# Optimization experiments

Hardware: AMD Instinct MI355X
Metric: run time of the kernel (lower is better)

## Reference

```python
import jax, jax.numpy as jnp
import numpy as np

N_HEADS = 16

def setup_inputs() -> dict:
    key = jax.random.key(0)
    ks = jax.random.split(key, 5)
    B, T, D, L = 2, 2048, 1024, 128
    x = jax.random.normal(ks[0], (B, T, D), dtype=jnp.float32)
    w_q = jax.random.normal(ks[1], (D, D), dtype=jnp.float32) / np.sqrt(D)
    w_d = jax.random.normal(ks[2], (D, L), dtype=jnp.float32) / np.sqrt(D)
    w_k = jax.random.normal(ks[3], (L, D), dtype=jnp.float32) / np.sqrt(L)
    w_v = jax.random.normal(ks[4], (L, D), dtype=jnp.float32) / np.sqrt(L)
    mask = jnp.ones((B, T), dtype=jnp.int32)
    return {"x": x, "mask": mask, "w_q": w_q, "w_d": w_d, "w_k": w_k, "w_v": w_v}


def reference(x, mask, w_q, w_d, w_k, w_v):
    B, T, D = x.shape
    H = N_HEADS
    dh = D // H
    q = x @ w_q                      # [B,T,D]
    latent = x @ w_d                 # [B,T,L]
    k = latent @ w_k                 # [B,T,D]
    v = latent @ w_v                 # [B,T,D]

    def split(t):
        return t.reshape(B, T, H, dh).transpose(0, 2, 1, 3)  # [B,H,T,dh]

    q, k, v = split(q), split(k), split(v)
    scores = jnp.einsum('bhqd,bhkd->bhqk', q, k) / jnp.sqrt(jnp.float32(dh))
    causal = jnp.tril(jnp.ones((T, T), dtype=bool))          # [T,T]
    keep = causal[None, None, :, :] & (mask[:, None, None, :] != 0)
    scores = jnp.where(keep, scores, jnp.float32(-jnp.inf))
    probs = jax.nn.softmax(scores, axis=-1)
    out = jnp.einsum('bhqk,bhkd->bhqd', probs, v)            # [B,H,T,dh]
    return out.transpose(0, 2, 1, 3).reshape(B, T, D)
```

## Files before the change

### kernel.cpp

```cpp
#include <hip/hip_runtime.h>

typedef __attribute__((ext_vector_type(8))) short bf16x8;
typedef __attribute__((ext_vector_type(4))) float f32x4;
typedef __attribute__((ext_vector_type(4))) unsigned u32x4;

__device__ inline unsigned short f2bf(float f) {
  unsigned u = __builtin_bit_cast(unsigned, f);
  unsigned r = u + 0x7FFFu + ((u >> 16) & 1u);
  return (unsigned short)(r >> 16);
}
__device__ inline float bf2f(unsigned short s) {
  unsigned u = ((unsigned)s) << 16;
  return __builtin_bit_cast(float, u);
}
__device__ inline float fexp2(float x) { return __builtin_amdgcn_exp2f(x); }

__device__ inline void gload_lds16(const unsigned short* g, unsigned short* l) {
  __builtin_amdgcn_global_load_lds(
      (const __attribute__((address_space(1))) unsigned int*)g,
      (__attribute__((address_space(3))) unsigned int*)l, 16, 0, 0);
}

__device__ __host__ inline int pv_perm(int k) {
  return ((k >> 5) & 1) * 32 + ((k >> 2) & 3) * 8 + ((k >> 4) & 1) * 4 + (k & 3);
}

__global__ __launch_bounds__(256) void prep_kernel(
    const float* __restrict__ x, const int* __restrict__ mask,
    const float* __restrict__ w_q, const float* __restrict__ w_d,
    const float* __restrict__ w_k, const float* __restrict__ w_v,
    unsigned short* __restrict__ x_bf, unsigned short* __restrict__ wqdt,
    unsigned short* __restrict__ wkvt, float* __restrict__ bias,
    int* __restrict__ tileok) {
  int bid = blockIdx.x;
  if (bid < 1024) {
    int base = bid * 4096 + threadIdx.x * 4;
#pragma unroll
    for (int it = 0; it < 4; ++it) {
      int idx = base + it * 1024;
      float4 v = *(const float4*)&x[idx];
      ushort4 o;
      o.x = f2bf(v.x); o.y = f2bf(v.y); o.z = f2bf(v.z); o.w = f2bf(v.w);
      *(ushort4*)&x_bf[idx] = o;
    }
    return;
  }
  int tb = bid - 1024;
  if (tb >= 1408) {
    int i = (tb - 1408) * 256 + threadIdx.x;
    int mv = mask[i];
    bias[i] = mv ? 0.0f : -1e30f;
    int ok = __all(mv != 0);
    if ((threadIdx.x & 63) == 0) tileok[i >> 6] = ok;
    return;
  }
  const float* in; unsigned short* out; int R, C, tr, tc;
  if (tb < 1024)      { in = w_q; out = wqdt;               R = 1024; C = 1024; tr = tb >> 5; tc = tb & 31; }
  else if (tb < 1152) { int t2 = tb - 1024; in = w_d; out = wqdt + 1024 * 1024; R = 1024; C = 128; tr = t2 >> 2; tc = t2 & 3; }
  else if (tb < 1280) { int t2 = tb - 1152; in = w_k; out = wkvt;               R = 128; C = 1024; tr = t2 >> 5; tc = t2 & 31; }
  else                { int t2 = tb - 1280; in = w_v; out = wkvt + 1024 * 128;  R = 128; C = 1024; tr = t2 >> 5; tc = t2 & 31; }
  __shared__ float t[32][33];
  int r0 = tr * 32, c0 = tc * 32;
  int tx = threadIdx.x & 31, ty = threadIdx.x >> 5;
  for (int r = ty; r < 32; r += 8)
    t[r][tx] = in[(size_t)(r0 + r) * C + c0 + tx];
  __syncthreads();
  for (int cc = ty; cc < 32; cc += 8)
    out[(size_t)(c0 + cc) * R + r0 + tx] = f2bf(t[tx][cc]);
}

template <int BN>
__global__ __launch_bounds__(256) void gemm_bt(const unsigned short* __restrict__ A, int lda,
                                               const unsigned short* __restrict__ Bt, int ldb,
                                               unsigned short* __restrict__ C, int ldc,
                                               int K) {
  constexpr int WM = (BN == 128) ? 2 : 4;
  constexpr int WN = 4 / WM;
  constexpr int MR = 128 / WM / 16;
  constexpr int NR = BN / WN / 16;
  constexpr int RPW = 128 / WM;
  constexpr int CPW = BN / WN;
  __shared__ unsigned short As[128 * 32];
  __shared__ unsigned short Bs[BN * 32];
  int m0 = blockIdx.x * 128, n0 = blockIdx.y * BN;
  int tid = threadIdx.x, w = tid >> 6, l = tid & 63;
  int lr = l & 15, lg = l >> 4;
  int wr = w / WN, wc = w % WN;
  f32x4 acc[MR][NR] = {};

  for (int k0 = 0; k0 < K; k0 += 32) {
    __syncthreads();
#pragma unroll
    for (int it = 0; it < 2; ++it) {
      int c = w * 2 + it;
      int row = c * 16 + (l >> 2);
      int col = (l & 3) * 8;
      gload_lds16(&A[(size_t)(m0 + row) * lda + k0 + col], &As[c * 512 + l * 8]);
    }
    if constexpr (BN == 128) {
#pragma unroll
      for (int it = 0; it < 2; ++it) {
        int c = w * 2 + it;
        int row = c * 16 + (l >> 2);
        int col = (l & 3) * 8;
        gload_lds16(&Bt[(size_t)(n0 + row) * ldb + k0 + col], &Bs[c * 512 + l * 8]);
      }
    } else {
      int row = w * 16 + (l >> 2);
      int col = (l & 3) * 8;
      gload_lds16(&Bt[(size_t)(n0 + row) * ldb + k0 + col], &Bs[w * 512 + l * 8]);
    }
    __syncthreads();
    bf16x8 af[MR], bfr[NR];
#pragma unroll
    for (int m = 0; m < MR; ++m)
      af[m] = *(const bf16x8*)&As[(wr * RPW + m * 16 + lr) * 32 + lg * 8];
#pragma unroll
    for (int n = 0; n < NR; ++n)
      bfr[n] = *(const bf16x8*)&Bs[(wc * CPW + n * 16 + lr) * 32 + lg * 8];
    __builtin_amdgcn_s_setprio(1);
#pragma unroll
    for (int m = 0; m < MR; ++m)
#pragma unroll
      for (int n = 0; n < NR; ++n)
        acc[m][n] = __builtin_amdgcn_mfma_f32_16x16x32_bf16(af[m], bfr[n], acc[m][n], 0, 0, 0);
    __builtin_amdgcn_s_setprio(0);
  }

#pragma unroll
  for (int m = 0; m < MR; ++m)
#pragma unroll
    for (int n = 0; n < NR; ++n)
#pragma unroll
      for (int i = 0; i < 4; ++i)
        C[(size_t)(m0 + wr * RPW + m * 16 + lg * 4 + i) * ldc + n0 + wc * CPW + n * 16 + lr] =
            f2bf(acc[m][n][i]);
}

__global__ __launch_bounds__(256) void gemm_kv(const unsigned short* __restrict__ A,
                                               const unsigned short* __restrict__ Bt,
                                               unsigned short* __restrict__ kvK,
                                               unsigned short* __restrict__ vt) {
  __shared__ unsigned short As[128 * 32];
  __shared__ unsigned short Bs[128 * 32];
  int m0 = blockIdx.x * 128, n0 = blockIdx.y * 128;
  int tid = threadIdx.x, w = tid >> 6, l = tid & 63;
  int lr = l & 15, lg = l >> 4;
  int wr = w >> 1, wc = w & 1;
  f32x4 acc[4][4] = {};

  for (int k0 = 0; k0 < 128; k0 += 32) {
    __syncthreads();
#pragma unroll
    for (int it = 0; it < 2; ++it) {
      int c = w * 2 + it;
      int row = c * 16 + (l >> 2);
      int col = (l & 3) * 8;
      gload_lds16(&A[(size_t)(m0 + row) * 1152 + k0 + col], &As[c * 512 + l * 8]);
      gload_lds16(&Bt[(size_t)(n0 + row) * 128 + k0 + col], &Bs[c * 512 + l * 8]);
    }
    __syncthreads();
    bf16x8 af[4], bfr[4];
#pragma unroll
    for (int m = 0; m < 4; ++m)
      af[m] = *(const bf16x8*)&As[(wr * 64 + m * 16 + lr) * 32 + lg * 8];
#pragma unroll
    for (int n = 0; n < 4; ++n)
      bfr[n] = *(const bf16x8*)&Bs[(wc * 64 + n * 16 + lr) * 32 + lg * 8];
    __builtin_amdgcn_s_setprio(1);
#pragma unroll
    for (int m = 0; m < 4; ++m)
#pragma unroll
      for (int n = 0; n < 4; ++n)
        acc[m][n] = __builtin_amdgcn_mfma_f32_16x16x32_bf16(af[m], bfr[n], acc[m][n], 0, 0, 0);
    __builtin_amdgcn_s_setprio(0);
  }

  if (blockIdx.y < 8) {
#pragma unroll
    for (int m = 0; m < 4; ++m)
#pragma unroll
      for (int n = 0; n < 4; ++n)
#pragma unroll
        for (int i = 0; i < 4; ++i)
          kvK[(size_t)(m0 + wr * 64 + m * 16 + lg * 4 + i) * 2048 + n0 + wc * 64 + n * 16 + lr] =
              f2bf(acc[m][n][i]);
  } else {
#pragma unroll
    for (int m = 0; m < 4; ++m)
#pragma unroll
      for (int n = 0; n < 4; ++n) {
        int vc = n0 - 1024 + wc * 64 + n * 16 + lr;
        int hh = vc >> 6, dd = vc & 63;
        int row0 = m0 + wr * 64 + m * 16 + lg * 4;
        int bb = row0 >> 11, t0 = row0 & 2047;
        size_t vrow = (size_t)((bb * 16 + hh) * 64 + dd);
        int slot = (t0 >> 6) * 64 + pv_perm(t0 & 63);
        ushort4 o;
        o.x = f2bf(acc[m][n][0]); o.y = f2bf(acc[m][n][1]);
        o.z = f2bf(acc[m][n][2]); o.w = f2bf(acc[m][n][3]);
        *(ushort4*)&vt[vrow * 2048 + slot] = o;
      }
  }
}

__global__ __launch_bounds__(512, 2) void attn_kernel(const unsigned short* __restrict__ qg,
                                                      const unsigned short* __restrict__ kvg,
                                                      const unsigned short* __restrict__ vtg,
                                                      const float* __restrict__ biasg,
                                                      const int* __restrict__ tileokg,
                                                      float* __restrict__ outg) {
  const int bh = blockIdx.x, qh = blockIdx.y;
  const int b = bh >> 4, h = bh & 15;
  const int tid = threadIdx.x, w = tid >> 6, l = tid & 63;
  const int lr = l & 15, lg = l >> 4;
  const int srow = tid >> 3, sc8 = (tid & 7) * 8;

  __shared__ unsigned short Ks[2][64 * 72];
  __shared__ unsigned short Vs[2][64 * 72];

  const float QSCALE = 0.125f * 1.44269504089f;

  for (int bi = 0; bi < 2; ++bi) {
    const int band = bi ? (15 - qh) : qh;
    const int NT = 2 * band + 2;
    const int qrow0 = band * 128 + w * 16;

    bf16x8 qf[2];
#pragma unroll
    for (int ks = 0; ks < 2; ++ks) {
      bf16x8 raw = *(const bf16x8*)&qg[(size_t)(b * 2048 + qrow0 + lr) * 1152 + h * 64 + ks * 32 + lg * 8];
#pragma unroll
      for (int j = 0; j < 8; ++j)
        raw[j] = (short)f2bf(bf2f((unsigned short)raw[j]) * QSCALE);
      qf[ks] = raw;
    }

    f32x4 acc[4] = {};
    float m_i = -1e30f, l_part = 0.f;

    bf16x8 kreg = *(const bf16x8*)&kvg[(size_t)(b * 2048 + srow) * 2048 + h * 64 + sc8];
    bf16x8 vreg = *(const bf16x8*)&vtg[((size_t)(bh * 64 + srow)) * 2048 + sc8];
    __syncthreads();
    *(bf16x8*)&Ks[0][srow * 72 + sc8] = kreg;
    *(bf16x8*)&Vs[0][srow * 72 + sc8] = vreg;
    __syncthreads();
    int cur = 0;

    for (int kt = 0; kt < NT; ++kt) {
      if (kt + 1 < NT) {
        kreg = *(const bf16x8*)&kvg[(size_t)(b * 2048 + (kt + 1) * 64 + srow) * 2048 + h * 64 + sc8];
        vreg = *(const bf16x8*)&vtg[((size_t)(bh * 64 + srow)) * 2048 + (kt + 1) * 64 + sc8];
      }

      const int d = kt - 2 * band;
      const bool skip = (d == 1) && (w < 4);
      if (!skip) {
        const bool isdiag = (d == 0 && w < 4) || (d == 1 && w >= 4);
        const int dlim = (w & 3) * 16 + lr;

        f32x4 s[4];
        __builtin_amdgcn_s_setprio(1);
#pragma unroll
        for (int n = 0; n < 4; ++n) {
          bf16x8 kf0 = *(const bf16x8*)&Ks[cur][(n * 16 + lr) * 72 + lg * 8];
          bf16x8 kf1 = *(const bf16x8*)&Ks[cur][(n * 16 + lr) * 72 + 32 + lg * 8];
          f32x4 z = {};
          z = __builtin_amdgcn_mfma_f32_16x16x32_bf16(kf0, qf[0], z, 0, 0, 0);
          z = __builtin_amdgcn_mfma_f32_16x16x32_bf16(kf1, qf[1], z, 0, 0, 0);
          s[n] = z;
        }
        __builtin_amdgcn_s_setprio(0);

        const int tok = tileokg[b * 32 + kt];
        float mx = -1e30f;
        if (tok) {
          if (isdiag) {
#pragma unroll
            for (int n = 0; n < 4; ++n)
#pragma unroll
              for (int i = 0; i < 4; ++i) {
                float v = (n * 16 + lg * 4 + i <= dlim) ? s[n][i] : -1e30f;
                s[n][i] = v;
                mx = fmaxf(mx, v);
              }
          } else {
#pragma unroll
            for (int n = 0; n < 4; ++n)
#pragma unroll
              for (int i = 0; i < 4; ++i)
                mx = fmaxf(mx, s[n][i]);
          }
        } else {
#pragma unroll
          for (int n = 0; n < 4; ++n)
#pragma unroll
            for (int i = 0; i < 4; ++i) {
              int keyl = n * 16 + lg * 4 + i;
              float v = s[n][i] + biasg[b * 2048 + kt * 64 + keyl];
              if (isdiag) v = (keyl <= dlim) ? v : -1e30f;
              s[n][i] = v;
              mx = fmaxf(mx, v);
            }
        }
        mx = fmaxf(mx, __shfl_xor(mx, 16, 64));
        mx = fmaxf(mx, __shfl_xor(mx, 32, 64));

        if (__any(mx - m_i > 8.0f)) {
          float mn = fmaxf(m_i, mx);
          float sc = fexp2(m_i - mn);
          m_i = mn;
          l_part *= sc;
          float scb[4];
#pragma unroll
          for (int i = 0; i < 4; ++i) scb[i] = __shfl(sc, lg * 4 + i, 64);
#pragma unroll
          for (int dt = 0; dt < 4; ++dt)
#pragma unroll
            for (int i = 0; i < 4; ++i) acc[dt][i] *= scb[i];
        }

        float rs = 0.f;
#pragma unroll
        for (int n = 0; n < 4; ++n)
#pragma unroll
          for (int i = 0; i < 4; ++i) {
            float e = fexp2(s[n][i] - m_i);
            s[n][i] = e;
            rs += e;
          }
        l_part += rs;

        unsigned pk[4][2];
#pragma unroll
        for (int n = 0; n < 4; ++n) {
          asm("v_cvt_pk_bf16_f32 %0, %1, %2" : "=v"(pk[n][0]) : "v"(s[n][0]), "v"(s[n][1]));
          asm("v_cvt_pk_bf16_f32 %0, %1, %2" : "=v"(pk[n][1]) : "v"(s[n][2]), "v"(s[n][3]));
        }
        bf16x8 paf[2];
#pragma unroll
        for (int ks = 0; ks < 2; ++ks) {
          u32x4 uv;
          uv[0] = pk[2 * ks][0];
          uv[1] = pk[2 * ks][1];
          uv[2] = pk[2 * ks + 1][0];
          uv[3] = pk[2 * ks + 1][1];
          paf[ks] = __builtin_bit_cast(bf16x8, uv);
        }

        __builtin_amdgcn_s_setprio(1);
#pragma unroll
        for (int ks = 0; ks < 2; ++ks)
#pragma unroll
          for (int dt = 0; dt < 4; ++dt) {
            bf16x8 vf = *(const bf16x8*)&Vs[cur][(dt * 16 + lr) * 72 + ks * 32 + lg * 8];
            acc[dt] = __builtin_amdgcn_mfma_f32_16x16x32_bf16(paf[ks], vf, acc[dt], 0, 0, 0);
          }
        __builtin_amdgcn_s_setprio(0);
      }

      if (kt + 1 < NT) {
        *(bf16x8*)&Ks[cur ^ 1][srow * 72 + sc8] = kreg;
        *(bf16x8*)&Vs[cur ^ 1][srow * 72 + sc8] = vreg;
        __syncthreads();
        cur ^= 1;
      }
    }

    float lt = l_part;
    lt += __shfl_xor(lt, 16, 64);
    lt += __shfl_xor(lt, 32, 64);
    float inv = 1.f / lt;
    float invb[4];
#pragma unroll
    for (int i = 0; i < 4; ++i) invb[i] = __shfl(inv, lg * 4 + i, 64);
#pragma unroll
    for (int dt = 0; dt < 4; ++dt)
#pragma unroll
      for (int i = 0; i < 4; ++i)
        outg[(size_t)(b * 2048 + qrow0 + lg * 4 + i) * 1024 + h * 64 + dt * 16 + lr] =
            acc[dt][i] * invb[i];
  }
}

extern "C" void kernel_launch(void* const* d_in, const int* in_sizes, int n_in,
                              void* d_out, int out_size, void* d_ws, size_t ws_size,
                              hipStream_t stream) {
  const float* x    = (const float*)d_in[0];
  const int*   mask = (const int*)d_in[1];
  const float* w_q  = (const float*)d_in[2];
  const float* w_d  = (const float*)d_in[3];
  const float* w_k  = (const float*)d_in[4];
  const float* w_v  = (const float*)d_in[5];
  float* out = (float*)d_out;

  char* ws = (char*)d_ws;
  size_t off = 0;
  auto alloc = [&](size_t elems) {
    unsigned short* p = (unsigned short*)(ws + off);
    off += ((elems * 2 + 255) & ~(size_t)255);
    return p;
  };
  unsigned short* x_bf = alloc(4194304);
  unsigned short* wqdt = alloc(1152 * 1024);
  unsigned short* wkvt = alloc(2048 * 128);
  unsigned short* qlat = alloc(4096 * 1152);
  unsigned short* kv   = alloc(4096 * 2048);
  unsigned short* vt   = alloc(4194304);
  float* bias = (float*)alloc(8192);
  int* tileok = (int*)alloc(128);

  prep_kernel<<<2448, 256, 0, stream>>>(x, mask, w_q, w_d, w_k, w_v, x_bf, wqdt, wkvt, bias, tileok);

  gemm_bt<64><<<dim3(32, 18), 256, 0, stream>>>(x_bf, 1024, wqdt, 1024, qlat, 1152, 1024);
  gemm_kv<<<dim3(32, 16), 256, 0, stream>>>(qlat + 1024, wkvt, kv, vt);

  attn_kernel<<<dim3(32, 8), 512, 0, stream>>>(qlat, kv, vt, bias, tileok, out);
}
```

Measured before the change: 84.23 us.

## Shrink attention blocks to 64-row bands and deepen Q-GEMM K-step

The attention kernel now uses 256-thread blocks, each handling two paired 64-row query bands instead of two 128-row bands, on a grid twice as large. This removes the wasted half-diagonal tile and the per-wave skip logic, and it balances causal work in finer pieces. Each thread now stages two K/V chunks per tile. The Q-projection GEMM is specialised into gemm_q, which loads a 64-wide K slab per sync (two 32-wide LDS panels) to halve the number of barriers. The cost is extra LDS use and more register pressure.

```diff
diff --git a/kernel.cpp b/kernel.cpp
--- a/kernel.cpp
+++ b/kernel.cpp
@@ -69,71 +69,59 @@
     out[(size_t)(c0 + cc) * R + r0 + tx] = f2bf(t[tx][cc]);
 }
 
-template <int BN>
-__global__ __launch_bounds__(256) void gemm_bt(const unsigned short* __restrict__ A, int lda,
-                                               const unsigned short* __restrict__ Bt, int ldb,
-                                               unsigned short* __restrict__ C, int ldc,
-                                               int K) {
-  constexpr int WM = (BN == 128) ? 2 : 4;
-  constexpr int WN = 4 / WM;
-  constexpr int MR = 128 / WM / 16;
-  constexpr int NR = BN / WN / 16;
-  constexpr int RPW = 128 / WM;
-  constexpr int CPW = BN / WN;
-  __shared__ unsigned short As[128 * 32];
-  __shared__ unsigned short Bs[BN * 32];
-  int m0 = blockIdx.x * 128, n0 = blockIdx.y * BN;
+__global__ __launch_bounds__(256) void gemm_q(const unsigned short* __restrict__ A,
+                                              const unsigned short* __restrict__ Bt,
+                                              unsigned short* __restrict__ C) {
+  __shared__ unsigned short As[2][128 * 32];
+  __shared__ unsigned short Bs[2][64 * 32];
+  int m0 = blockIdx.x * 128, n0 = blockIdx.y * 64;
   int tid = threadIdx.x, w = tid >> 6, l = tid & 63;
   int lr = l & 15, lg = l >> 4;
-  int wr = w / WN, wc = w % WN;
-  f32x4 acc[MR][NR] = {};
-
-  for (int k0 = 0; k0 < K; k0 += 32) {
-    __syncthreads();
+  f32x4 acc[2][4] = {};
+
+  for (int k0 = 0; k0 < 1024; k0 += 64) {
+    __syncthreads();
+#pragma unroll
+    for (int it = 0; it < 4; ++it) {
+      int s = w * 4 + it;
+      int p = s >> 3, c = s & 7;
+      int row = c * 16 + (l >> 2), col = (l & 3) * 8;
+      gload_lds16(&A[(size_t)(m0 + row) * 1024 + k0 + p * 32 + col], &As[p][c * 512 + l * 8]);
+    }
 #pragma unroll
     for (int it = 0; it < 2; ++it) {
-      int c = w * 2 + it;
-      int row = c * 16 + (l >> 2);
-      int col = (l & 3) * 8;
-      gload_lds16(&A[(size_t)(m0 + row) * lda + k0 + col], &As[c * 512 + l * 8]);
-    }
-    if constexpr (BN == 128) {
-#pragma unroll
-      for (int it = 0; it < 2; ++it) {
-        int c = w * 2 + it;
-        int row = c * 16 + (l >> 2);
-        int col = (l & 3) * 8;
-        gload_lds16(&Bt[(size_t)(n0 + row) * ldb + k0 + col], &Bs[c * 512 + l * 8]);
-      }
-    } else {
-      int row = w * 16 + (l >> 2);
-      int col = (l & 3) * 8;
-      gload_lds16(&Bt[(size_t)(n0 + row) * ldb + k0 + col], &Bs[w * 512 + l * 8]);
-    }
-    __syncthreads();
-    bf16x8 af[MR], bfr[NR];
-#pragma unroll
-    for (int m = 0; m < MR; ++m)
-      af[m] = *(const bf16x8*)&As[(wr * RPW + m * 16 + lr) * 32 + lg * 8];
-#pragma unroll
-    for (int n = 0; n < NR; ++n)
-      bfr[n] = *(const bf16x8*)&Bs[(wc * CPW + n * 16 + lr) * 32 + lg * 8];
-    __builtin_amdgcn_s_setprio(1);
-#pragma unroll
-    for (int m = 0; m < MR; ++m)
-#pragma unroll
-      for (int n = 0; n < NR; ++n)
-        acc[m][n] = __builtin_amdgcn_mfma_f32_16x16x32_bf16(af[m], bfr[n], acc[m][n], 0, 0, 0);
-    __builtin_amdgcn_s_setprio(0);
-  }
-
-#pragma unroll
-  for (int m = 0; m < MR; ++m)
-#pragma unroll
-    for (int n = 0; n < NR; ++n)
+      int s = w * 2 + it;
+      int p = s >> 2, c = s & 3;
+      int row = c * 16 + (l >> 2), col = (l & 3) * 8;
+      gload_lds16(&Bt[(size_t)(n0 + row) * 1024 + k0 + p * 32 + col], &Bs[p][c * 512 + l * 8]);
+    }
+    __syncthreads();
+#pragma unroll
+    for (int p = 0; p < 2; ++p) {
+      bf16x8 af[2], bfr[4];
+#pragma unroll
+      for (int m = 0; m < 2; ++m)
+        af[m] = *(const bf16x8*)&As[p][(w * 32 + m * 16 + lr) * 32 + lg * 8];
+#pragma unroll
+      for (int n = 0; n < 4; ++n)
+        bfr[n] = *(const bf16x8*)&Bs[p][(n * 16 + lr) * 32 + lg * 8];
+      __builtin_amdgcn_s_setprio(1);
+#pragma unroll
+      for (int m = 0; m < 2; ++m)
+#pragma unroll
+        for (int n = 0; n < 4; ++n)
+          acc[m][n] = __builtin_amdgcn_mfma_f32_16x16x32_bf16(af[m], bfr[n], acc[m][n], 0, 0, 0);
+      __builtin_amdgcn_s_setprio(0);
+    }
+  }
+
+#pragma unroll
+  for (int m = 0; m < 2; ++m)
+#pragma unroll
+    for (int n = 0; n < 4; ++n)
 #pragma unroll
       for (int i = 0; i < 4; ++i)
-        C[(size_t)(m0 + wr * RPW + m * 16 + lg * 4 + i) * ldc + n0 + wc * CPW + n * 16 + lr] =
+        C[(size_t)(m0 + w * 32 + m * 16 + lg * 4 + i) * 1152 + n0 + n * 16 + lr] =
             f2bf(acc[m][n][i]);
 }
 
@@ -204,17 +192,16 @@
   }
 }
 
-__global__ __launch_bounds__(512, 2) void attn_kernel(const unsigned short* __restrict__ qg,
+__global__ __launch_bounds__(256, 2) void attn_kernel(const unsigned short* __restrict__ qg,
                                                       const unsigned short* __restrict__ kvg,
                                                       const unsigned short* __restrict__ vtg,
                                                       const float* __restrict__ biasg,
                                                       const int* __restrict__ tileokg,
                                                       float* __restrict__ outg) {
-  const int bh = blockIdx.x, qh = blockIdx.y;
+  const int bh = blockIdx.x, pr = blockIdx.y;
   const int b = bh >> 4, h = bh & 15;
   const int tid = threadIdx.x, w = tid >> 6, l = tid & 63;
   const int lr = l & 15, lg = l >> 4;
-  const int srow = tid >> 3, sc8 = (tid & 7) * 8;
 
   __shared__ unsigned short Ks[2][64 * 72];
   __shared__ unsigned short Vs[2][64 * 72];
@@ -222,9 +209,9 @@
   const float QSCALE = 0.125f * 1.44269504089f;
 
   for (int bi = 0; bi < 2; ++bi) {
-    const int band = bi ? (15 - qh) : qh;
-    const int NT = 2 * band + 2;
-    const int qrow0 = band * 128 + w * 16;
+    const int band = bi ? (31 - pr) : pr;
+    const int NT = band + 1;
+    const int qrow0 = band * 64 + w * 16;
 
     bf16x8 qf[2];
 #pragma unroll
@@ -239,129 +226,142 @@
     f32x4 acc[4] = {};
     float m_i = -1e30f, l_part = 0.f;
 
-    bf16x8 kreg = *(const bf16x8*)&kvg[(size_t)(b * 2048 + srow) * 2048 + h * 64 + sc8];
-    bf16x8 vreg = *(const bf16x8*)&vtg[((size_t)(bh * 64 + srow)) * 2048 + sc8];
-    __syncthreads();
-    *(bf16x8*)&Ks[0][srow * 72 + sc8] = kreg;
-    *(bf16x8*)&Vs[0][srow * 72 + sc8] = vreg;
+    bf16x8 kreg[2], vreg[2];
+#pragma unroll
+    for (int it = 0; it < 2; ++it) {
+      int slot = it * 256 + tid, row = slot >> 3, c8 = (slot & 7) * 8;
+      kreg[it] = *(const bf16x8*)&kvg[(size_t)(b * 2048 + row) * 2048 + h * 64 + c8];
+      vreg[it] = *(const bf16x8*)&vtg[((size_t)(bh * 64 + row)) * 2048 + c8];
+    }
+    __syncthreads();
+#pragma unroll
+    for (int it = 0; it < 2; ++it) {
+      int slot = it * 256 + tid, row = slot >> 3, c8 = (slot & 7) * 8;
+      *(bf16x8*)&Ks[0][row * 72 + c8] = kreg[it];
+      *(bf16x8*)&Vs[0][row * 72 + c8] = vreg[it];
+    }
     __syncthreads();
     int cur = 0;
 
     for (int kt = 0; kt < NT; ++kt) {
       if (kt + 1 < NT) {
-        kreg = *(const bf16x8*)&kvg[(size_t)(b * 2048 + (kt + 1) * 64 + srow) * 2048 + h * 64 + sc8];
-        vreg = *(const bf16x8*)&vtg[((size_t)(bh * 64 + srow)) * 2048 + (kt + 1) * 64 + sc8];
-      }
-
-      const int d = kt - 2 * band;
-      const bool skip = (d == 1) && (w < 4);
-      if (!skip) {
-        const bool isdiag = (d == 0 && w < 4) || (d == 1 && w >= 4);
-        const int dlim = (w & 3) * 16 + lr;
-
-        f32x4 s[4];
-        __builtin_amdgcn_s_setprio(1);
-#pragma unroll
-        for (int n = 0; n < 4; ++n) {
-          bf16x8 kf0 = *(const bf16x8*)&Ks[cur][(n * 16 + lr) * 72 + lg * 8];
-          bf16x8 kf1 = *(const bf16x8*)&Ks[cur][(n * 16 + lr) * 72 + 32 + lg * 8];
-          f32x4 z = {};
-          z = __builtin_amdgcn_mfma_f32_16x16x32_bf16(kf0, qf[0], z, 0, 0, 0);
-          z = __builtin_amdgcn_mfma_f32_16x16x32_bf16(kf1, qf[1], z, 0, 0, 0);
-          s[n] = z;
+#pragma unroll
+        for (int it = 0; it < 2; ++it) {
+          int slot = it * 256 + tid, row = slot >> 3, c8 = (slot & 7) * 8;
+          kreg[it] = *(const bf16x8*)&kvg[(size_t)(b * 2048 + (kt + 1) * 64 + row) * 2048 + h * 64 + c8];
+          vreg[it] = *(const bf16x8*)&vtg[((size_t)(bh * 64 + row)) * 2048 + (kt + 1) * 64 + c8];
         }
-        __builtin_amdgcn_s_setprio(0);
-
-        const int tok = tileokg[b * 32 + kt];
-        float mx = -1e30f;
-        if (tok) {
-          if (isdiag) {
-#pragma unroll
-            for (int n = 0; n < 4; ++n)
-#pragma unroll
-              for (int i = 0; i < 4; ++i) {
-                float v = (n * 16 + lg * 4 + i <= dlim) ? s[n][i] : -1e30f;
-                s[n][i] = v;
-                mx = fmaxf(mx, v);
-              }
-          } else {
-#pragma unroll
-            for (int n = 0; n < 4; ++n)
-#pragma unroll
-              for (int i = 0; i < 4; ++i)
-                mx = fmaxf(mx, s[n][i]);
-          }
-        } else {
+      }
+
+      const bool diag = (kt == NT - 1);
+      const int dlim = w * 16 + lr;
+
+      f32x4 s[4];
+      __builtin_amdgcn_s_setprio(1);
+#pragma unroll
+      for (int n = 0; n < 4; ++n) {
+        bf16x8 kf0 = *(const bf16x8*)&Ks[cur][(n * 16 + lr) * 72 + lg * 8];
+        bf16x8 kf1 = *(const bf16x8*)&Ks[cur][(n * 16 + lr) * 72 + 32 + lg * 8];
+        f32x4 z = {};
+        z = __builtin_amdgcn_mfma_f32_16x16x32_bf16(kf0, qf[0], z, 0, 0, 0);
+        z = __builtin_amdgcn_mfma_f32_16x16x32_bf16(kf1, qf[1], z, 0, 0, 0);
+        s[n] = z;
+      }
+      __builtin_amdgcn_s_setprio(0);
+
+      const int tok = tileokg[b * 32 + kt];
+      float mx = -1e30f;
+      if (tok) {
+        if (diag) {
 #pragma unroll
           for (int n = 0; n < 4; ++n)
 #pragma unroll
             for (int i = 0; i < 4; ++i) {
-              int keyl = n * 16 + lg * 4 + i;
-              float v = s[n][i] + biasg[b * 2048 + kt * 64 + keyl];
-              if (isdiag) v = (keyl <= dlim) ? v : -1e30f;
+              float v = (n * 16 + lg * 4 + i <= dlim) ? s[n][i] : -1e30f;
               s[n][i] = v;
               mx = fmaxf(mx, v);
             }
+        } else {
+#pragma unroll
+          for (int n = 0; n < 4; ++n)
+#pragma unroll
+            for (int i = 0; i < 4; ++i)
+              mx = fmaxf(mx, s[n][i]);
         }
-        mx = fmaxf(mx, __shfl_xor(mx, 16, 64));
-        mx = fmaxf(mx, __shfl_xor(mx, 32, 64));
-
-        if (__any(mx - m_i > 8.0f)) {
-          float mn = fmaxf(m_i, mx);
-          float sc = fexp2(m_i - mn);
-          m_i = mn;
-          l_part *= sc;
-          float scb[4];
-#pragma unroll
-          for (int i = 0; i < 4; ++i) scb[i] = __shfl(sc, lg * 4 + i, 64);
-#pragma unroll
-          for (int dt = 0; dt < 4; ++dt)
-#pragma unroll
-            for (int i = 0; i < 4; ++i) acc[dt][i] *= scb[i];
+      } else {
+#pragma unroll
+        for (int n = 0; n < 4; ++n)
+#pragma unroll
+          for (int i = 0; i < 4; ++i) {
+            int keyl = n * 16 + lg * 4 + i;
+            float v = s[n][i] + biasg[b * 2048 + kt * 64 + keyl];
+            if (diag) v = (keyl <= dlim) ? v : -1e30f;
+            s[n][i] = v;
+            mx = fmaxf(mx, v);
+          }
+      }
+      mx = fmaxf(mx, __shfl_xor(mx, 16, 64));
+      mx = fmaxf(mx, __shfl_xor(mx, 32, 64));
+
+      if (__any(mx - m_i > 8.0f)) {
+        float mn = fmaxf(m_i, mx);
+        float sc = fexp2(m_i - mn);
+        m_i = mn;
+        l_part *= sc;
+        float scb[4];
+#pragma unroll
+        for (int i = 0; i < 4; ++i) scb[i] = __shfl(sc, lg * 4 + i, 64);
+#pragma unroll
+        for (int dt = 0; dt < 4; ++dt)
+#pragma unroll
+          for (int i = 0; i < 4; ++i) acc[dt][i] *= scb[i];
+      }
+
+      float rs = 0.f;
+#pragma unroll
+      for (int n = 0; n < 4; ++n)
+#pragma unroll
+        for (int i = 0; i < 4; ++i) {
+          float e = fexp2(s[n][i] - m_i);
+          s[n][i] = e;
+          rs += e;
         }
-
-        float rs = 0.f;
-#pragma unroll
-        for (int n = 0; n < 4; ++n)
-#pragma unroll
-          for (int i = 0; i < 4; ++i) {
-            float e = fexp2(s[n][i] - m_i);
-            s[n][i] = e;
-            rs += e;
-          }
-        l_part += rs;
-
-        unsigned pk[4][2];
-#pragma unroll
-        for (int n = 0; n < 4; ++n) {
-          asm("v_cvt_pk_bf16_f32 %0, %1, %2" : "=v"(pk[n][0]) : "v"(s[n][0]), "v"(s[n][1]));
-          asm("v_cvt_pk_bf16_f32 %0, %1, %2" : "=v"(pk[n][1]) : "v"(s[n][2]), "v"(s[n][3]));
+      l_part += rs;
+
+      unsigned pk[4][2];
+#pragma unroll
+      for (int n = 0; n < 4; ++n) {
+        asm("v_cvt_pk_bf16_f32 %0, %1, %2" : "=v"(pk[n][0]) : "v"(s[n][0]), "v"(s[n][1]));
+        asm("v_cvt_pk_bf16_f32 %0, %1, %2" : "=v"(pk[n][1]) : "v"(s[n][2]), "v"(s[n][3]));
+      }
+      bf16x8 paf[2];
+#pragma unroll
+      for (int ks = 0; ks < 2; ++ks) {
+        u32x4 uv;
+        uv[0] = pk[2 * ks][0];
+        uv[1] = pk[2 * ks][1];
+        uv[2] = pk[2 * ks + 1][0];
+        uv[3] = pk[2 * ks + 1][1];
+        paf[ks] = __builtin_bit_cast(bf16x8, uv);
+      }
+
+      __builtin_amdgcn_s_setprio(1);
+#pragma unroll
+      for (int ks = 0; ks < 2; ++ks)
+#pragma unroll
+        for (int dt = 0; dt < 4; ++dt) {
+          bf16x8 vf = *(const bf16x8*)&Vs[cur][(dt * 16 + lr) * 72 + ks * 32 + lg * 8];
+          acc[dt] = __builtin_amdgcn_mfma_f32_16x16x32_bf16(paf[ks], vf, acc[dt], 0, 0, 0);
         }
-        bf16x8 paf[2];
-#pragma unroll
-        for (int ks = 0; ks < 2; ++ks) {
-          u32x4 uv;
-          uv[0] = pk[2 * ks][0];
-          uv[1] = pk[2 * ks][1];
-          uv[2] = pk[2 * ks + 1][0];
-          uv[3] = pk[2 * ks + 1][1];
-          paf[ks] = __builtin_bit_cast(bf16x8, uv);
+      __builtin_amdgcn_s_setprio(0);
+
+      if (kt + 1 < NT) {
+#pragma unroll
+        for (int it = 0; it < 2; ++it) {
+          int slot = it * 256 + tid, row = slot >> 3, c8 = (slot & 7) * 8;
+          *(bf16x8*)&Ks[cur ^ 1][row * 72 + c8] = kreg[it];
+          *(bf16x8*)&Vs[cur ^ 1][row * 72 + c8] = vreg[it];
         }
-
-        __builtin_amdgcn_s_setprio(1);
-#pragma unroll
-        for (int ks = 0; ks < 2; ++ks)
-#pragma unroll
-          for (int dt = 0; dt < 4; ++dt) {
-            bf16x8 vf = *(const bf16x8*)&Vs[cur][(dt * 16 + lr) * 72 + ks * 32 + lg * 8];
-            acc[dt] = __builtin_amdgcn_mfma_f32_16x16x32_bf16(paf[ks], vf, acc[dt], 0, 0, 0);
-          }
-        __builtin_amdgcn_s_setprio(0);
-      }
-
-      if (kt + 1 < NT) {
-        *(bf16x8*)&Ks[cur ^ 1][srow * 72 + sc8] = kreg;
-        *(bf16x8*)&Vs[cur ^ 1][srow * 72 + sc8] = vreg;
         __syncthreads();
         cur ^= 1;
       }
@@ -412,8 +412,8 @@
 
   prep_kernel<<<2448, 256, 0, stream>>>(x, mask, w_q, w_d, w_k, w_v, x_bf, wqdt, wkvt, bias, tileok);
 
-  gemm_bt<64><<<dim3(32, 18), 256, 0, stream>>>(x_bf, 1024, wqdt, 1024, qlat, 1152, 1024);
+  gemm_q<<<dim3(32, 18), 256, 0, stream>>>(x_bf, wqdt, qlat);
   gemm_kv<<<dim3(32, 16), 256, 0, stream>>>(qlat + 1024, wkvt, kv, vt);
 
-  attn_kernel<<<dim3(32, 8), 512, 0, stream>>>(qlat, kv, vt, bias, tileok, out);
-}
+  attn_kernel<<<dim3(32, 16), 256, 0, stream>>>(qlat, kv, vt, bias, tileok, out);
+}
```

Result: faster. 74.75 us (-11.3%).
